# Kernel optimization log

Hardware: AMD Instinct MI355X
Metric: run time of the kernel (lower is better)

The kernel has to match this reference:

```python
import jax, jax.numpy as jnp
import numpy as np
from jax import lax

GAMMA = 1.0

def _conv(x, w, b, stride, pad):
    y = lax.conv_general_dilated(x, w, (stride, stride), [(pad, pad), (pad, pad)],
                                 dimension_numbers=('NCHW', 'OIHW', 'NCHW'))
    return y + b[None, :, None, None]

def _maxpool2s1(x):
    return lax.reduce_window(x, -jnp.inf, lax.max, (1, 1, 2, 2), (1, 1, 1, 1), 'VALID')

def setup_inputs() -> dict:
    key = jax.random.key(0)
    ks = jax.random.split(key, 13)
    d = {}
    d['x'] = jax.random.normal(ks[0], (128, 3, 250, 250), dtype=jnp.float32)
    d['conv1_w'] = jax.random.normal(ks[1], (6, 3, 5, 5), dtype=jnp.float32) / np.sqrt(3 * 25)
    d['conv1_b'] = jax.random.normal(ks[2], (6,), dtype=jnp.float32) * 0.01
    d['conv2_w'] = jax.random.normal(ks[3], (15, 6, 3, 3), dtype=jnp.float32) / np.sqrt(6 * 9)
    d['conv2_b'] = jax.random.normal(ks[4], (15,), dtype=jnp.float32) * 0.01
    d['fc1_w'] = jax.random.normal(ks[5], (120, 55815), dtype=jnp.float32) / np.sqrt(55815.0)
    d['fc1_b'] = jax.random.normal(ks[6], (120,), dtype=jnp.float32) * 0.01
    d['fc2_w'] = jax.random.normal(ks[7], (84, 120), dtype=jnp.float32) / np.sqrt(120.0)
    d['fc2_b'] = jax.random.normal(ks[8], (84,), dtype=jnp.float32) * 0.01
    d['fc3_w'] = jax.random.normal(ks[9], (1, 84), dtype=jnp.float32) / np.sqrt(84.0)
    d['fc3_b'] = jax.random.normal(ks[10], (1,), dtype=jnp.float32) * 0.01
    d['support'] = jax.random.normal(ks[11], (10, 1), dtype=jnp.float32)
    return d

def reference(x, conv1_w, conv1_b, conv2_w, conv2_b, fc1_w, fc1_b, fc2_w, fc2_b, fc3_w, fc3_b, support):
    h = jax.nn.relu(_conv(x, conv1_w, conv1_b, 2, 1))   # [B,6,124,124]
    h = _maxpool2s1(h)                                   # [B,6,123,123] (dropout = identity in eval)
    h = jax.nn.relu(_conv(h, conv2_w, conv2_b, 2, 1))    # [B,15,62,62]
    h = _maxpool2s1(h)                                   # [B,15,61,61]
    h = h.reshape(h.shape[0], -1)                        # [B,55815]
    h = jax.nn.relu(h @ fc1_w.T + fc1_b)
    h = jax.nn.relu(h @ fc2_w.T + fc2_b)
    h = h @ fc3_w.T + fc3_b                              # [B,1]
    # fused RBF kernel vs support set: k[i,j] = exp(-gamma*(x_i - s_j)^2)
    diff = h - support[:, 0][None, :]                    # [B,10]
    k = jnp.exp(-GAMMA * diff * diff)
    h = k.mean(axis=1, keepdims=True)                    # [B,1]
    probs = jax.nn.sigmoid(h)
    return jnp.concatenate((probs, 1.0 - probs), axis=-1)  # [B,2]
```

## Files before the change

### kernel.cpp

```cpp
#include <hip/hip_runtime.h>
#include <math.h>


#define BATCH 128

#define C1_ST 78
#define C1_COLS 69
#define C1_ROWS 67
#define C1_TOT (C1_ROWS * C1_COLS)
__global__ __launch_bounds__(256) void conv1_pool_kernel(
    const float* __restrict__ x, const float* __restrict__ w,
    const float* __restrict__ bias, float* __restrict__ out) {
  const int b = blockIdx.z;
  const int P0 = blockIdx.x * 32;
  const int R0 = blockIdx.y * 31;
  const int tid = threadIdx.x;
  const int t = tid >> 3;
  const int s = tid & 7;

  __shared__ float lds[C1_ROWS * C1_ST];
  float* cbuf = lds;

  float acc[5][6];
#pragma unroll
  for (int oc = 0; oc < 6; oc++) {
    float bv = bias[oc];
#pragma unroll
    for (int dc = 0; dc < 5; dc++) acc[dc][oc] = bv;
  }

  const int ihb = 2 * R0 - 1, iwb = 2 * P0 - 1;

#pragma unroll 1
  for (int ci = 0; ci < 3; ci++) {
    __syncthreads();
    const float* src = x + (size_t)(b * 3 + ci) * 62500;
#pragma unroll 1
    for (int base = tid; base < C1_TOT; base += 1024) {
      float vv[4];
      int lrv[4], ilv[4];
#pragma unroll
      for (int k = 0; k < 4; k++) {
        int i = base + (k << 8);
        int lr = (int)(((unsigned)i * 121575u) >> 23);
        int il = i - lr * 69;
        lrv[k] = lr; ilv[k] = il;
        int ih = ihb + lr, iw = iwb + il;
        bool ok = (i < C1_TOT) && ((unsigned)ih < 250u) && ((unsigned)iw < 250u);
        vv[k] = ok ? src[ih * 250 + iw] : 0.f;
      }
#pragma unroll
      for (int k = 0; k < 4; k++) {
        int i = base + (k << 8);
        if (i < C1_TOT) lds[lrv[k] * C1_ST + ilv[k] + (ilv[k] >> 3)] = vv[k];
      }
    }
    __syncthreads();

    const float* rbase = &lds[(2 * t) * C1_ST + 9 * s];
#pragma unroll
    for (int ir = 0; ir < 5; ir++) {
      const float* rpl = rbase + ir * C1_ST;
      const float* rph = rpl + 1;
      float v[13];
#pragma unroll
      for (int j = 0; j < 8; j++)  v[j] = rpl[j];
#pragma unroll
      for (int j = 8; j < 13; j++) v[j] = rph[j];
#pragma unroll
      for (int oc = 0; oc < 6; oc++) {
        const float* wr = w + ((oc * 3 + ci) * 5 + ir) * 5;
        float w0 = wr[0], w1 = wr[1], w2 = wr[2], w3 = wr[3], w4 = wr[4];
#pragma unroll
        for (int dc = 0; dc < 5; dc++) {
          float a = acc[dc][oc];
          a += w0 * v[2 * dc + 0];
          a += w1 * v[2 * dc + 1];
          a += w2 * v[2 * dc + 2];
          a += w3 * v[2 * dc + 3];
          a += w4 * v[2 * dc + 4];
          acc[dc][oc] = a;
        }
      }
    }
  }

  __syncthreads();
  if (t == 8 || t == 16 || t == 24) {
    float* cb = &cbuf[(((t >> 3) - 1) * 8 + s) * 30];
#pragma unroll
    for (int oc = 0; oc < 6; oc++)
#pragma unroll
      for (int dc = 0; dc < 5; dc++) cb[oc * 5 + dc] = acc[dc][oc];
  }
  __syncthreads();

  const int p0 = R0 + t;
  const int c0 = P0 + 4 * s;
  const bool edge = ((t & 7) == 7) && (t < 31);
  const bool wr_ok = (t < 31) && (p0 < 123);
  const float* cb = &cbuf[((t >> 3) * 8 + s) * 30];

#pragma unroll
  for (int oc = 0; oc < 6; oc++) {
    float a0 = acc[0][oc], a1 = acc[1][oc], a2 = acc[2][oc],
          a3 = acc[3][oc], a4 = acc[4][oc];
    float n0 = __shfl_down(a0, 8), n1 = __shfl_down(a1, 8),
          n2 = __shfl_down(a2, 8), n3 = __shfl_down(a3, 8),
          n4 = __shfl_down(a4, 8);
    if (edge) {
      n0 = cb[oc * 5 + 0]; n1 = cb[oc * 5 + 1]; n2 = cb[oc * 5 + 2];
      n3 = cb[oc * 5 + 3]; n4 = cb[oc * 5 + 4];
    }
    if (wr_ok) {
      float* orow = out + ((size_t)(b * 6 + oc) * 123 + p0) * 123;
      float m0 = fmaxf(fmaxf(fmaxf(a0, a1), fmaxf(n0, n1)), 0.f);
      float m1 = fmaxf(fmaxf(fmaxf(a1, a2), fmaxf(n1, n2)), 0.f);
      float m2 = fmaxf(fmaxf(fmaxf(a2, a3), fmaxf(n2, n3)), 0.f);
      float m3 = fmaxf(fmaxf(fmaxf(a3, a4), fmaxf(n3, n4)), 0.f);
      if (c0 + 3 < 123) {
        *(float4*)&orow[c0] = make_float4(m0, m1, m2, m3);
      } else {
        if (c0 < 123) orow[c0] = m0;
        if (c0 + 1 < 123) orow[c0 + 1] = m1;
        if (c0 + 2 < 123) orow[c0 + 2] = m2;
      }
    }
  }
}

#define C2_ST 84
#define C2_TOT (35 * 67)
__global__ __launch_bounds__(256) void conv2_pool_kernel(
    const float* __restrict__ in, const float* __restrict__ w,
    const float* __restrict__ bias, float* __restrict__ out) {
  const int b = blockIdx.z;
  const int P0 = blockIdx.x * 32;
  const int R0 = blockIdx.y * 16;
  const int tid = threadIdx.x;
  const int t = tid >> 4;
  const int s = tid & 15;

  __shared__ float lds[35 * C2_ST];

  const int ihb = 2 * R0 - 1, iwb = 2 * P0 - 1;
  const int r = R0 + t;
  const int c0 = P0 + 2 * s;

#pragma unroll 1
  for (int ocg = 0; ocg < 2; ocg++) {
    const int oc0 = ocg * 7;
    float acc0[3][8], acc1[3][8];
#pragma unroll
    for (int k = 0; k < 8; k++) {
      float bv = bias[oc0 + k];
#pragma unroll
      for (int dc = 0; dc < 3; dc++) { acc0[dc][k] = bv; acc1[dc][k] = bv; }
    }

#pragma unroll 1
    for (int ci = 0; ci < 6; ci++) {
      __syncthreads();
      const float* src = in + (size_t)(b * 6 + ci) * 15129;
#pragma unroll 1
      for (int base = tid; base < C2_TOT; base += 2048) {
        float vv[8];
        int lrv[8], ilv[8];
#pragma unroll
        for (int k = 0; k < 8; k++) {
          int i = base + (k << 8);
          int lr = (int)(((unsigned)i * 125204u) >> 23);
          int il = i - lr * 67;
          lrv[k] = lr; ilv[k] = il;
          int ih = ihb + lr, iw = iwb + il;
          bool ok = (i < C2_TOT) && ((unsigned)ih < 123u) && ((unsigned)iw < 123u);
          vv[k] = ok ? src[ih * 123 + iw] : 0.f;
        }
#pragma unroll
        for (int k = 0; k < 8; k++) {
          int i = base + (k << 8);
          if (i < C2_TOT) lds[lrv[k] * C2_ST + ilv[k] + (ilv[k] >> 2)] = vv[k];
        }
      }
      __syncthreads();

#pragma unroll 1
      for (int ir = 0; ir < 5; ir++) {
        const float* rp = &lds[(2 * t + ir) * C2_ST + 5 * s];
        float v[7];
#pragma unroll
        for (int j = 0; j < 7; j++) v[j] = rp[j + (j >> 2)];

        if (ir < 3) {
#pragma unroll
          for (int k = 0; k < 8; k++) {
            const float* wr = w + (((oc0 + k) * 6 + ci) * 3 + ir) * 3;
            float w0 = wr[0], w1 = wr[1], w2 = wr[2];
#pragma unroll
            for (int dc = 0; dc < 3; dc++) {
              float a = acc0[dc][k];
              a += w0 * v[2 * dc + 0];
              a += w1 * v[2 * dc + 1];
              a += w2 * v[2 * dc + 2];
              acc0[dc][k] = a;
            }
          }
        }
        if (ir >= 2) {
#pragma unroll
          for (int k = 0; k < 8; k++) {
            const float* wr = w + (((oc0 + k) * 6 + ci) * 3 + (ir - 2)) * 3;
            float w0 = wr[0], w1 = wr[1], w2 = wr[2];
#pragma unroll
            for (int dc = 0; dc < 3; dc++) {
              float a = acc1[dc][k];
              a += w0 * v[2 * dc + 0];
              a += w1 * v[2 * dc + 1];
              a += w2 * v[2 * dc + 2];
              acc1[dc][k] = a;
            }
          }
        }
      }
    }

    if (r < 61) {
#pragma unroll
      for (int k = 0; k < 8; k++) {
        int oc = oc0 + k;
        float* orow = out + ((size_t)(b * 15 + oc) * 61 + r) * 61;
        float m0 = fmaxf(fmaxf(fmaxf(acc0[0][k], acc0[1][k]),
                               fmaxf(acc1[0][k], acc1[1][k])), 0.f);
        float m1 = fmaxf(fmaxf(fmaxf(acc0[1][k], acc0[2][k]),
                               fmaxf(acc1[1][k], acc1[2][k])), 0.f);
        if (c0 + 1 < 61) {
          *(float2*)&orow[c0] = make_float2(m0, m1);
        } else if (c0 < 61) {
          orow[c0] = m0;
        }
      }
    }
  }
}

#define KTOT 55815
#define NPART 512
#define KCHUNK 112
__global__ __launch_bounds__(512) void fc1_splitk_kernel(
    const float* __restrict__ act, const float* __restrict__ w,
    float* __restrict__ partial) {
  const int kbase = blockIdx.x * KCHUNK;
  const int tid = threadIdx.x;
  const int tx = tid & 31, ty = tid >> 5;
  __shared__ float ldsA[8 * 132];
  __shared__ float ldsB[8 * 132];
  float acc[8][4];
#pragma unroll
  for (int i = 0; i < 8; i++)
#pragma unroll
    for (int j = 0; j < 4; j++) acc[i][j] = 0.f;

  for (int s8 = 0; s8 < KCHUNK / 8; s8++) {
    int kofs = kbase + s8 * 8;
    __syncthreads();
    for (int i = tid; i < 1024; i += 512) {
      int m = i >> 3, kk = i & 7;
      int k = kofs + kk;
      ldsA[kk * 132 + m] = (k < KTOT) ? act[m * KTOT + k] : 0.f;
    }
    for (int i = tid; i < 960; i += 512) {
      int n = i >> 3, kk = i & 7;
      int k = kofs + kk;
      ldsB[kk * 132 + n] = (k < KTOT) ? w[n * KTOT + k] : 0.f;
    }
    __syncthreads();
#pragma unroll
    for (int kk = 0; kk < 8; kk++) {
      float4 a0 = *(const float4*)&ldsA[kk * 132 + ty * 8];
      float4 a1 = *(const float4*)&ldsA[kk * 132 + ty * 8 + 4];
      float4 b0 = *(const float4*)&ldsB[kk * 132 + tx * 4];
      float av[8] = {a0.x, a0.y, a0.z, a0.w, a1.x, a1.y, a1.z, a1.w};
      float bv[4] = {b0.x, b0.y, b0.z, b0.w};
#pragma unroll
      for (int i = 0; i < 8; i++)
#pragma unroll
        for (int j = 0; j < 4; j++) acc[i][j] += av[i] * bv[j];
    }
  }

  if (tx < 30) {
    float* dst = partial + (size_t)blockIdx.x * 15360;
#pragma unroll
    for (int i = 0; i < 8; i++) {
      int row = ty * 8 + i;
      float4 st = make_float4(acc[i][0], acc[i][1], acc[i][2], acc[i][3]);
      *(float4*)&dst[row * 120 + tx * 4] = st;
    }
  }
}

__global__ __launch_bounds__(256) void fc1_reduce_kernel(
    const float* __restrict__ partial, const float* __restrict__ bias,
    float* __restrict__ h1) {
  const int g = threadIdx.x >> 5, il = threadIdx.x & 31;
  const int idx = blockIdx.x * 32 + il;
  const float* p = partial + (size_t)g * 15360 + idx;
  float s = 0.f;
#pragma unroll 8
  for (int q = 0; q < 64; q++) s += p[(size_t)(q * 8) * 15360];
  __shared__ float red[8][32];
  red[g][il] = s;
  __syncthreads();
  if (threadIdx.x < 32) {
    float tsum = 0.f;
#pragma unroll
    for (int gg = 0; gg < 8; gg++) tsum += red[gg][threadIdx.x];
    h1[idx] = fmaxf(tsum + bias[idx % 120], 0.f);
  }
}

__global__ __launch_bounds__(128) void head_kernel(
    const float* __restrict__ h1, const float* __restrict__ fc2_w,
    const float* __restrict__ fc2_b, const float* __restrict__ fc3_w,
    const float* __restrict__ fc3_b, const float* __restrict__ support,
    float* __restrict__ out) {
  int b = blockIdx.x, t = threadIdx.x;
  __shared__ float hrow[120];
  __shared__ float s2[84];
  if (t < 120) hrow[t] = h1[b * 120 + t];
  __syncthreads();
  if (t < 84) {
    float d = fc2_b[t];
    for (int k = 0; k < 120; k++) d += fc2_w[t * 120 + k] * hrow[k];
    s2[t] = fmaxf(d, 0.f);
  }
  __syncthreads();
  if (t == 0) {
    float h = fc3_b[0];
    for (int j = 0; j < 84; j++) h += fc3_w[j] * s2[j];
    float ks = 0.f;
    for (int j = 0; j < 10; j++) {
      float diff = h - support[j];
      ks += expf(-diff * diff);
    }
    ks *= 0.1f;
    float p = 1.f / (1.f + expf(-ks));
    out[b * 2] = p;
    out[b * 2 + 1] = 1.f - p;
  }
}

extern "C" void kernel_launch(void* const* d_in, const int* in_sizes, int n_in,
                              void* d_out, int out_size, void* d_ws, size_t ws_size,
                              hipStream_t stream) {
  const float* x   = (const float*)d_in[0];
  const float* c1w = (const float*)d_in[1];
  const float* c1b = (const float*)d_in[2];
  const float* c2w = (const float*)d_in[3];
  const float* c2b = (const float*)d_in[4];
  const float* f1w = (const float*)d_in[5];
  const float* f1b = (const float*)d_in[6];
  const float* f2w = (const float*)d_in[7];
  const float* f2b = (const float*)d_in[8];
  const float* f3w = (const float*)d_in[9];
  const float* f3b = (const float*)d_in[10];
  const float* sup = (const float*)d_in[11];
  float* out = (float*)d_out;

  char* ws = (char*)d_ws;
  float* pool1 = (float*)ws;
  float* act   = (float*)(ws + 46476288);
  float* part  = (float*)ws;
  float* h1    = (float*)(ws + 33000000);

  conv1_pool_kernel<<<dim3(4, 4, BATCH), 256, 0, stream>>>(x, c1w, c1b, pool1);
  conv2_pool_kernel<<<dim3(2, 4, BATCH), 256, 0, stream>>>(pool1, c2w, c2b, act);
  fc1_splitk_kernel<<<NPART, 512, 0, stream>>>(act, f1w, part);
  fc1_reduce_kernel<<<480, 256, 0, stream>>>(part, f1b, h1);
  head_kernel<<<BATCH, 128, 0, stream>>>(h1, f2w, f2b, f3w, f3b, sup, out);
}
```

Baseline: 349.8 us.

## Compute all conv2 channels per block, pad activation rows, widen fc1 k-step

Conv2 now accumulates all 15 output channels in one pass, so each input tile is staged into LDS once instead of twice. The cost is many more accumulator registers, which may lower occupancy. Conv2 output rows are padded to a 16-byte-aligned stride (KPAD), letting fc1 read activations as float4. fc1 also stages 16 k values per step instead of 8, halving the number of barriers.

```diff
diff --git a/kernel.cpp b/kernel.cpp
--- a/kernel.cpp
+++ b/kernel.cpp
@@ -3,6 +3,7 @@
 
 
 #define BATCH 128
+#define KPAD 55816
 
 #define C1_ST 78
 #define C1_COLS 69
@@ -147,97 +148,91 @@
   const int r = R0 + t;
   const int c0 = P0 + 2 * s;
 
-#pragma unroll 1
-  for (int ocg = 0; ocg < 2; ocg++) {
-    const int oc0 = ocg * 7;
-    float acc0[3][8], acc1[3][8];
-#pragma unroll
-    for (int k = 0; k < 8; k++) {
-      float bv = bias[oc0 + k];
-#pragma unroll
-      for (int dc = 0; dc < 3; dc++) { acc0[dc][k] = bv; acc1[dc][k] = bv; }
-    }
-
-#pragma unroll 1
-    for (int ci = 0; ci < 6; ci++) {
-      __syncthreads();
-      const float* src = in + (size_t)(b * 6 + ci) * 15129;
-#pragma unroll 1
-      for (int base = tid; base < C2_TOT; base += 2048) {
-        float vv[8];
-        int lrv[8], ilv[8];
-#pragma unroll
-        for (int k = 0; k < 8; k++) {
-          int i = base + (k << 8);
-          int lr = (int)(((unsigned)i * 125204u) >> 23);
-          int il = i - lr * 67;
-          lrv[k] = lr; ilv[k] = il;
-          int ih = ihb + lr, iw = iwb + il;
-          bool ok = (i < C2_TOT) && ((unsigned)ih < 123u) && ((unsigned)iw < 123u);
-          vv[k] = ok ? src[ih * 123 + iw] : 0.f;
-        }
-#pragma unroll
-        for (int k = 0; k < 8; k++) {
-          int i = base + (k << 8);
-          if (i < C2_TOT) lds[lrv[k] * C2_ST + ilv[k] + (ilv[k] >> 2)] = vv[k];
-        }
-      }
-      __syncthreads();
-
-#pragma unroll 1
-      for (int ir = 0; ir < 5; ir++) {
-        const float* rp = &lds[(2 * t + ir) * C2_ST + 5 * s];
-        float v[7];
-#pragma unroll
-        for (int j = 0; j < 7; j++) v[j] = rp[j + (j >> 2)];
-
-        if (ir < 3) {
-#pragma unroll
-          for (int k = 0; k < 8; k++) {
-            const float* wr = w + (((oc0 + k) * 6 + ci) * 3 + ir) * 3;
-            float w0 = wr[0], w1 = wr[1], w2 = wr[2];
-#pragma unroll
-            for (int dc = 0; dc < 3; dc++) {
-              float a = acc0[dc][k];
-              a += w0 * v[2 * dc + 0];
-              a += w1 * v[2 * dc + 1];
-              a += w2 * v[2 * dc + 2];
-              acc0[dc][k] = a;
-            }
+  float acc0[3][15], acc1[3][15];
+#pragma unroll
+  for (int oc = 0; oc < 15; oc++) {
+    float bv = bias[oc];
+#pragma unroll
+    for (int dc = 0; dc < 3; dc++) { acc0[dc][oc] = bv; acc1[dc][oc] = bv; }
+  }
+
+#pragma unroll 1
+  for (int ci = 0; ci < 6; ci++) {
+    __syncthreads();
+    const float* src = in + (size_t)(b * 6 + ci) * 15129;
+#pragma unroll 1
+    for (int base = tid; base < C2_TOT; base += 1024) {
+      float vv[4];
+      int ladr[4];
+#pragma unroll
+      for (int k = 0; k < 4; k++) {
+        int i = base + (k << 8);
+        int lr = (int)(((unsigned)i * 125204u) >> 23);
+        int il = i - lr * 67;
+        int ih = ihb + lr, iw = iwb + il;
+        bool ok = (i < C2_TOT) && ((unsigned)ih < 123u) && ((unsigned)iw < 123u);
+        vv[k] = ok ? src[ih * 123 + iw] : 0.f;
+        ladr[k] = (i < C2_TOT) ? (lr * C2_ST + il + (il >> 2)) : -1;
+      }
+#pragma unroll
+      for (int k = 0; k < 4; k++) {
+        if (ladr[k] >= 0) lds[ladr[k]] = vv[k];
+      }
+    }
+    __syncthreads();
+
+#pragma unroll 1
+    for (int ir = 0; ir < 5; ir++) {
+      const float* rp = &lds[(2 * t + ir) * C2_ST + 5 * s];
+      float v[7];
+#pragma unroll
+      for (int j = 0; j < 7; j++) v[j] = rp[j + (j >> 2)];
+
+      if (ir < 3) {
+#pragma unroll
+        for (int oc = 0; oc < 15; oc++) {
+          const float* wr = w + ((oc * 6 + ci) * 3 + ir) * 3;
+          float w0 = wr[0], w1 = wr[1], w2 = wr[2];
+#pragma unroll
+          for (int dc = 0; dc < 3; dc++) {
+            float a = acc0[dc][oc];
+            a += w0 * v[2 * dc + 0];
+            a += w1 * v[2 * dc + 1];
+            a += w2 * v[2 * dc + 2];
+            acc0[dc][oc] = a;
           }
         }
-        if (ir >= 2) {
-#pragma unroll
-          for (int k = 0; k < 8; k++) {
-            const float* wr = w + (((oc0 + k) * 6 + ci) * 3 + (ir - 2)) * 3;
-            float w0 = wr[0], w1 = wr[1], w2 = wr[2];
-#pragma unroll
-            for (int dc = 0; dc < 3; dc++) {
-              float a = acc1[dc][k];
-              a += w0 * v[2 * dc + 0];
-              a += w1 * v[2 * dc + 1];
-              a += w2 * v[2 * dc + 2];
-              acc1[dc][k] = a;
-            }
+      }
+      if (ir >= 2) {
+#pragma unroll
+        for (int oc = 0; oc < 15; oc++) {
+          const float* wr = w + ((oc * 6 + ci) * 3 + (ir - 2)) * 3;
+          float w0 = wr[0], w1 = wr[1], w2 = wr[2];
+#pragma unroll
+          for (int dc = 0; dc < 3; dc++) {
+            float a = acc1[dc][oc];
+            a += w0 * v[2 * dc + 0];
+            a += w1 * v[2 * dc + 1];
+            a += w2 * v[2 * dc + 2];
+            acc1[dc][oc] = a;
           }
         }
       }
     }
-
-    if (r < 61) {
-#pragma unroll
-      for (int k = 0; k < 8; k++) {
-        int oc = oc0 + k;
-        float* orow = out + ((size_t)(b * 15 + oc) * 61 + r) * 61;
-        float m0 = fmaxf(fmaxf(fmaxf(acc0[0][k], acc0[1][k]),
-                               fmaxf(acc1[0][k], acc1[1][k])), 0.f);
-        float m1 = fmaxf(fmaxf(fmaxf(acc0[1][k], acc0[2][k]),
-                               fmaxf(acc1[1][k], acc1[2][k])), 0.f);
-        if (c0 + 1 < 61) {
-          *(float2*)&orow[c0] = make_float2(m0, m1);
-        } else if (c0 < 61) {
-          orow[c0] = m0;
-        }
+  }
+
+  if (r < 61) {
+#pragma unroll
+    for (int oc = 0; oc < 15; oc++) {
+      float* orow = out + (size_t)b * KPAD + (oc * 3721 + r * 61);
+      float m0 = fmaxf(fmaxf(fmaxf(acc0[0][oc], acc0[1][oc]),
+                             fmaxf(acc1[0][oc], acc1[1][oc])), 0.f);
+      float m1 = fmaxf(fmaxf(fmaxf(acc0[1][oc], acc0[2][oc]),
+                             fmaxf(acc1[1][oc], acc1[2][oc])), 0.f);
+      if (c0 + 1 < 61) {
+        *(float2*)&orow[c0] = make_float2(m0, m1);
+      } else if (c0 < 61) {
+        orow[c0] = m0;
       }
     }
   }
@@ -246,36 +241,51 @@
 #define KTOT 55815
 #define NPART 512
 #define KCHUNK 112
+#define KSTEP 16
 __global__ __launch_bounds__(512) void fc1_splitk_kernel(
     const float* __restrict__ act, const float* __restrict__ w,
     float* __restrict__ partial) {
   const int kbase = blockIdx.x * KCHUNK;
   const int tid = threadIdx.x;
   const int tx = tid & 31, ty = tid >> 5;
-  __shared__ float ldsA[8 * 132];
-  __shared__ float ldsB[8 * 132];
+  __shared__ float ldsA[KSTEP * 132];
+  __shared__ float ldsB[KSTEP * 132];
   float acc[8][4];
 #pragma unroll
   for (int i = 0; i < 8; i++)
 #pragma unroll
     for (int j = 0; j < 4; j++) acc[i][j] = 0.f;
 
-  for (int s8 = 0; s8 < KCHUNK / 8; s8++) {
-    int kofs = kbase + s8 * 8;
-    __syncthreads();
-    for (int i = tid; i < 1024; i += 512) {
-      int m = i >> 3, kk = i & 7;
-      int k = kofs + kk;
-      ldsA[kk * 132 + m] = (k < KTOT) ? act[m * KTOT + k] : 0.f;
-    }
-    for (int i = tid; i < 960; i += 512) {
-      int n = i >> 3, kk = i & 7;
+  const int mA = tid >> 2;
+  const int qA = (tid & 3) * 4;
+
+  for (int s16 = 0; s16 < KCHUNK / KSTEP; s16++) {
+    int kofs = kbase + s16 * KSTEP;
+    __syncthreads();
+    {
+      int k = kofs + qA;
+      float4 a4;
+      if (k + 3 < KTOT) {
+        a4 = *(const float4*)&act[(size_t)mA * KPAD + k];
+      } else {
+        a4.x = (k + 0 < KTOT) ? act[(size_t)mA * KPAD + k + 0] : 0.f;
+        a4.y = (k + 1 < KTOT) ? act[(size_t)mA * KPAD + k + 1] : 0.f;
+        a4.z = (k + 2 < KTOT) ? act[(size_t)mA * KPAD + k + 2] : 0.f;
+        a4.w = (k + 3 < KTOT) ? act[(size_t)mA * KPAD + k + 3] : 0.f;
+      }
+      ldsA[(qA + 0) * 132 + mA] = a4.x;
+      ldsA[(qA + 1) * 132 + mA] = a4.y;
+      ldsA[(qA + 2) * 132 + mA] = a4.z;
+      ldsA[(qA + 3) * 132 + mA] = a4.w;
+    }
+    for (int i = tid; i < 1920; i += 512) {
+      int n = i >> 4, kk = i & 15;
       int k = kofs + kk;
       ldsB[kk * 132 + n] = (k < KTOT) ? w[n * KTOT + k] : 0.f;
     }
     __syncthreads();
 #pragma unroll
-    for (int kk = 0; kk < 8; kk++) {
+    for (int kk = 0; kk < KSTEP; kk++) {
       float4 a0 = *(const float4*)&ldsA[kk * 132 + ty * 8];
       float4 a1 = *(const float4*)&ldsA[kk * 132 + ty * 8 + 4];
       float4 b0 = *(const float4*)&ldsB[kk * 132 + tx * 4];
```

Result: faster. 326.7 us (-6.6%).
